# Performance work log

Measured on AMD Instinct MI355X. Metric: run time of the kernel, lower is better.

## Reference

```python
import jax, jax.numpy as jnp
import numpy as np

N_NODES = 100352
NUM_GRAPHS = 512
NODES_PER_GRAPH = 196  # N_NODES / NUM_GRAPHS, equal-size graphs
N_EDGES = 1605632
IN_C, HID_C, OUT_C, K = 128, 64, 32, 30


def setup_inputs() -> dict:
    key = jax.random.key(0)
    ks = jax.random.split(key, 4)
    x = jax.random.normal(ks[0], (N_NODES, IN_C), dtype=jnp.float32)
    edge_index = jax.random.randint(ks[1], (2, N_EDGES), 0, N_NODES, dtype=jnp.int32)
    batch = jnp.repeat(jnp.arange(NUM_GRAPHS, dtype=jnp.int32), NODES_PER_GRAPH)
    W1 = jax.random.normal(ks[2], (IN_C, HID_C), jnp.float32) * (1.0 / np.sqrt(IN_C))
    b1 = jnp.zeros((HID_C,), jnp.float32)
    W2 = jax.random.normal(ks[3], (HID_C, OUT_C), jnp.float32) * (1.0 / np.sqrt(HID_C))
    b2 = jnp.zeros((OUT_C,), jnp.float32)
    return dict(x=x, edge_index=edge_index, batch=batch, W1=W1, b1=b1, W2=W2, b2=b2)


def gcn_conv(x, src, dst, W, b, num_nodes):
    # PyG GCNConv: xW, add self-loops, symmetric normalization, scatter-add to dst.
    xw = x @ W  # [N, D_out]
    deg = jax.ops.segment_sum(jnp.ones_like(dst, dtype=xw.dtype), dst,
                              num_segments=num_nodes) + 1.0  # +1 for self-loop
    dis = jax.lax.rsqrt(deg)  # deg^{-1/2}
    msg = (dis[src] * dis[dst])[:, None] * xw[src]  # [E, D_out]
    out = jax.ops.segment_sum(msg, dst, num_segments=num_nodes)
    out = out + (dis * dis)[:, None] * xw  # self-loop term deg^{-1} * xw
    return out + b


def sort_pool(x, batch, num_graphs, max_nodes, k):
    # PyG SortAggregation: dense per-graph batch, sort nodes desc by last channel, top-k, zero padding.
    N, D = x.shape
    fill = x.min() - 1.0
    counts = jax.ops.segment_sum(jnp.ones((N,), jnp.int32), batch, num_segments=num_graphs)
    starts = jnp.cumsum(counts) - counts  # exclusive prefix sum
    pos = jnp.arange(N, dtype=jnp.int32) - starts[batch]
    dense = jnp.full((num_graphs, max_nodes, D), fill, x.dtype).at[batch, pos].set(x)
    order = jnp.argsort(-dense[:, :, -1], axis=1)[:, :k]  # [B, k] top-k by last channel
    topk = jnp.take_along_axis(dense, order[:, :, None], axis=1)  # [B, k, D]
    topk = jnp.where(topk == fill, jnp.zeros((), x.dtype), topk)
    return topk.reshape(num_graphs, k * D)


def reference(x, edge_index, batch, W1, b1, W2, b2):
    src, dst = edge_index[0], edge_index[1]
    n = x.shape[0]
    h = jax.nn.relu(gcn_conv(x, src, dst, W1, b1, n))
    h = gcn_conv(h, src, dst, W2, b2, n)
    return sort_pool(h, batch, NUM_GRAPHS, NODES_PER_GRAPH, K)
```

## Files before the change

kernel.cpp:

```cpp
#include <hip/hip_runtime.h>

#define N_NODES   100352
#define N_EDGES   1605632
#define IN_C      128
#define HID_C     64
#define OUT_C     32
#define NUM_GRAPHS 512
#define NPG       196
#define TOPK      30

#define NB        196
#define BCAP      10240
#define LCAP      10240

typedef float v16f __attribute__((ext_vector_type(16)));

#define OFF_DEG     0u
#define OFF_ROWPTR  401408u
#define OFF_DIS     802816u
#define OFF_BCNT    1204224u
#define OFF_BBASE   1205248u
#define OFF_ARENA   1206272u
#define OFF_OUT2    1206272u
#define OFF_CSR     17262592u
#define OFF_XW1     23685120u
#define OFF_H       49375232u
#define OFF_XW2     75065344u

__global__ __launch_bounds__(256) void k_bucket(const int* __restrict__ src, const int* __restrict__ dst,
                                                int* __restrict__ bucket_cnt, int2* __restrict__ arena) {
    __shared__ int hist[NB];
    __shared__ int cur[NB];
    int tid = threadIdx.x;
    for (int i = tid; i < NB; i += 256) hist[i] = 0;
    __syncthreads();
    int e0 = (blockIdx.x * 256 + tid) * 8;
    int4 sa = ((const int4*)src)[e0 / 4], sb = ((const int4*)src)[e0 / 4 + 1];
    int4 da = ((const int4*)dst)[e0 / 4], db = ((const int4*)dst)[e0 / 4 + 1];
    int es[8] = {sa.x, sa.y, sa.z, sa.w, sb.x, sb.y, sb.z, sb.w};
    int ed[8] = {da.x, da.y, da.z, da.w, db.x, db.y, db.z, db.w};
    int eb[8];
#pragma unroll
    for (int j = 0; j < 8; ++j) { eb[j] = ed[j] >> 9; atomicAdd(&hist[eb[j]], 1); }
    __syncthreads();
    for (int i = tid; i < NB; i += 256) {
        int c = hist[i];
        cur[i] = (c > 0) ? atomicAdd(&bucket_cnt[i], c) : 0;
    }
    __syncthreads();
#pragma unroll
    for (int j = 0; j < 8; ++j) {
        int p = atomicAdd(&cur[eb[j]], 1);
        if (p < BCAP) arena[(size_t)eb[j] * BCAP + p] = make_int2(es[j], ed[j] & 511);
    }
}

__global__ __launch_bounds__(256) void k_bscan(const int* __restrict__ bucket_cnt, int* __restrict__ bucket_base) {
    __shared__ int s[256];
    int t = threadIdx.x;
    int v = (t < NB) ? bucket_cnt[t] : 0;
    s[t] = v;
    __syncthreads();
    for (int o = 1; o < 256; o <<= 1) {
        int a = (t >= o) ? s[t - o] : 0;
        __syncthreads();
        s[t] += a;
        __syncthreads();
    }
    if (t < NB) bucket_base[t] = s[t] - v;
}

__global__ __launch_bounds__(256) void k_build(const int2* __restrict__ arena, const int* __restrict__ bucket_cnt,
                                               const int* __restrict__ bucket_base, int* __restrict__ row_ptr,
                                               int* __restrict__ deg, float* __restrict__ dis,
                                               int* __restrict__ csr_src) {
    __shared__ int dloc[512];
    __shared__ int sc[512];
    __shared__ int cur[512];
    __shared__ int stage[LCAP];
    int b = blockIdx.x;
    int tid = threadIdx.x;
    int nb = min(bucket_cnt[b], BCAP);
    int gbase = bucket_base[b];
    const int2* ap = arena + (size_t)b * BCAP;
    for (int i = tid; i < 512; i += 256) dloc[i] = 0;
    __syncthreads();
    for (int i = tid; i < nb; i += 256) {
        int2 e = ap[i];
        atomicAdd(&dloc[e.y], 1);
    }
    __syncthreads();
    for (int i = tid; i < 512; i += 256) sc[i] = dloc[i];
    __syncthreads();
    for (int o = 1; o < 512; o <<= 1) {
        int i0 = tid, i1 = tid + 256;
        int v0 = (i0 >= o) ? sc[i0 - o] : 0;
        int v1 = (i1 >= o) ? sc[i1 - o] : 0;
        __syncthreads();
        sc[i0] += v0;
        sc[i1] += v1;
        __syncthreads();
    }
    for (int i = tid; i < 512; i += 256) {
        int d = dloc[i];
        int off = sc[i] - d;
        int node = b * 512 + i;
        row_ptr[node] = gbase + off;
        deg[node] = d;
        dis[node] = (float)(1.0 / sqrt((double)(d + 1)));
        cur[i] = off;
    }
    __syncthreads();
    bool inlds = (nb <= LCAP);
    for (int i = tid; i < nb; i += 256) {
        int2 e = ap[i];
        int p = atomicAdd(&cur[e.y], 1);
        if (inlds) stage[p] = e.x;
        else       csr_src[gbase + p] = e.x;
    }
    __syncthreads();
    if (inlds)
        for (int i = tid; i < nb; i += 256) csr_src[gbase + i] = stage[i];
}

__global__ __launch_bounds__(256) void k_mm1(const float* __restrict__ x, const float* __restrict__ W1,
                                             const float* __restrict__ dis, float* __restrict__ xw1s) {
    int tid = threadIdx.x;
    int n = blockIdx.x * 128 + (tid & 127);
    int ch = __builtin_amdgcn_readfirstlane((tid >> 7) * 32);
    const float4* xrow = (const float4*)(x + (size_t)n * IN_C);
    float acc[32];
#pragma unroll
    for (int c = 0; c < 32; ++c) acc[c] = 0.f;
    float4 xq = xrow[0];
#pragma unroll 1
    for (int q = 0; q < IN_C / 4; ++q) {
        float4 xn = xrow[(q + 1) & (IN_C / 4 - 1)];
        const float* wrow = W1 + q * 4 * HID_C + ch;
#pragma unroll
        for (int kk = 0; kk < 4; ++kk) {
            const float* wp = wrow + kk * HID_C;
            v16f w0, w1;
            asm volatile("s_load_dwordx16 %0, %1, 0x0"  : "=s"(w0) : "s"(wp));
            asm volatile("s_load_dwordx16 %0, %1, 0x40" : "=s"(w1) : "s"(wp));
            asm volatile("s_waitcnt lgkmcnt(0)" : "+s"(w0), "+s"(w1));
            float xk = (kk == 0) ? xq.x : (kk == 1) ? xq.y : (kk == 2) ? xq.z : xq.w;
#pragma unroll
            for (int c = 0; c < 16; ++c) {
                acc[c]      = fmaf(xk, w0[c], acc[c]);
                acc[c + 16] = fmaf(xk, w1[c], acc[c + 16]);
            }
        }
        xq = xn;
    }
    float dv = dis[n];
    float4* orow = (float4*)(xw1s + (size_t)n * HID_C + ch);
#pragma unroll
    for (int c4 = 0; c4 < 8; ++c4) {
        float4 o;
        o.x = acc[4 * c4 + 0] * dv;
        o.y = acc[4 * c4 + 1] * dv;
        o.z = acc[4 * c4 + 2] * dv;
        o.w = acc[4 * c4 + 3] * dv;
        orow[c4] = o;
    }
}

__global__ __launch_bounds__(256) void k_agg1(const float* __restrict__ xw1s, const int* __restrict__ csr_src,
                                              const int* __restrict__ row_ptr, const int* __restrict__ deg,
                                              const float* __restrict__ dis, const float* __restrict__ b1,
                                              float* __restrict__ h) {
    int lane = threadIdx.x & 63;
    int v = blockIdx.x * 4 + (threadIdx.x >> 6);
    int start = row_ptr[v];
    int cnt = deg[v];
    float acc0 = xw1s[(size_t)v * HID_C + lane];
    float acc1 = 0.f, acc2 = 0.f, acc3 = 0.f;
    for (int base = 0; base < cnt; base += 64) {
        int mcnt = min(64, cnt - base);
        int sj = 0;
        if (lane < mcnt) sj = csr_src[start + base + lane];
        int j = 0;
        for (; j + 8 <= mcnt; j += 8) {
            int s0 = __shfl(sj, j + 0), s1 = __shfl(sj, j + 1);
            int s2 = __shfl(sj, j + 2), s3 = __shfl(sj, j + 3);
            int s4 = __shfl(sj, j + 4), s5 = __shfl(sj, j + 5);
            int s6 = __shfl(sj, j + 6), s7 = __shfl(sj, j + 7);
            float v0 = xw1s[(size_t)s0 * HID_C + lane];
            float v1 = xw1s[(size_t)s1 * HID_C + lane];
            float v2 = xw1s[(size_t)s2 * HID_C + lane];
            float v3 = xw1s[(size_t)s3 * HID_C + lane];
            float v4 = xw1s[(size_t)s4 * HID_C + lane];
            float v5 = xw1s[(size_t)s5 * HID_C + lane];
            float v6 = xw1s[(size_t)s6 * HID_C + lane];
            float v7 = xw1s[(size_t)s7 * HID_C + lane];
            acc0 += v0 + v4;
            acc1 += v1 + v5;
            acc2 += v2 + v6;
            acc3 += v3 + v7;
        }
        for (; j < mcnt; ++j) {
            int s = __shfl(sj, j);
            acc0 += xw1s[(size_t)s * HID_C + lane];
        }
    }
    float o = fmaf(dis[v], (acc0 + acc1) + (acc2 + acc3), b1[lane]);
    h[(size_t)v * HID_C + lane] = fmaxf(o, 0.f);
}

__global__ __launch_bounds__(256) void k_mm2(const float* __restrict__ h, const float* __restrict__ W2,
                                             const float* __restrict__ dis, float* __restrict__ xw2s) {
    int tid = threadIdx.x;
    int n = blockIdx.x * 128 + (tid & 127);
    int ch = __builtin_amdgcn_readfirstlane((tid >> 7) * 16);
    const float4* hrow = (const float4*)(h + (size_t)n * HID_C);
    float acc[16];
#pragma unroll
    for (int c = 0; c < 16; ++c) acc[c] = 0.f;
    float4 xq = hrow[0];
#pragma unroll 1
    for (int q = 0; q < HID_C / 4; ++q) {
        float4 xn = hrow[(q + 1) & (HID_C / 4 - 1)];
        const float* wrow = W2 + q * 4 * OUT_C + ch;
#pragma unroll
        for (int kk = 0; kk < 4; ++kk) {
            const float* wp = wrow + kk * OUT_C;
            v16f w0;
            asm volatile("s_load_dwordx16 %0, %1, 0x0" : "=s"(w0) : "s"(wp));
            asm volatile("s_waitcnt lgkmcnt(0)" : "+s"(w0));
            float xk = (kk == 0) ? xq.x : (kk == 1) ? xq.y : (kk == 2) ? xq.z : xq.w;
#pragma unroll
            for (int c = 0; c < 16; ++c)
                acc[c] = fmaf(xk, w0[c], acc[c]);
        }
        xq = xn;
    }
    float dv = dis[n];
    float4* orow = (float4*)(xw2s + (size_t)n * OUT_C + ch);
#pragma unroll
    for (int c4 = 0; c4 < 4; ++c4) {
        float4 o;
        o.x = acc[4 * c4 + 0] * dv;
        o.y = acc[4 * c4 + 1] * dv;
        o.z = acc[4 * c4 + 2] * dv;
        o.w = acc[4 * c4 + 3] * dv;
        orow[c4] = o;
    }
}

__global__ __launch_bounds__(256) void k_agg2(const float* __restrict__ xw2s, const int* __restrict__ csr_src,
                                              const int* __restrict__ row_ptr, const int* __restrict__ deg,
                                              const float* __restrict__ dis, const float* __restrict__ b2,
                                              float* __restrict__ out2) {
    int lane = threadIdx.x & 31;
    int v = blockIdx.x * 8 + (threadIdx.x >> 5);
    int start = row_ptr[v];
    int cnt = deg[v];
    float acc0 = xw2s[(size_t)v * OUT_C + lane];
    float acc1 = 0.f, acc2 = 0.f, acc3 = 0.f;
    for (int base = 0; base < cnt; base += 32) {
        int mcnt = min(32, cnt - base);
        int sj = 0;
        if (lane < mcnt) sj = csr_src[start + base + lane];
        int j = 0;
        for (; j + 8 <= mcnt; j += 8) {
            int s0 = __shfl(sj, j + 0, 32), s1 = __shfl(sj, j + 1, 32);
            int s2 = __shfl(sj, j + 2, 32), s3 = __shfl(sj, j + 3, 32);
            int s4 = __shfl(sj, j + 4, 32), s5 = __shfl(sj, j + 5, 32);
            int s6 = __shfl(sj, j + 6, 32), s7 = __shfl(sj, j + 7, 32);
            float v0 = xw2s[(size_t)s0 * OUT_C + lane];
            float v1 = xw2s[(size_t)s1 * OUT_C + lane];
            float v2 = xw2s[(size_t)s2 * OUT_C + lane];
            float v3 = xw2s[(size_t)s3 * OUT_C + lane];
            float v4 = xw2s[(size_t)s4 * OUT_C + lane];
            float v5 = xw2s[(size_t)s5 * OUT_C + lane];
            float v6 = xw2s[(size_t)s6 * OUT_C + lane];
            float v7 = xw2s[(size_t)s7 * OUT_C + lane];
            acc0 += v0 + v4;
            acc1 += v1 + v5;
            acc2 += v2 + v6;
            acc3 += v3 + v7;
        }
        for (; j < mcnt; ++j) {
            int s = __shfl(sj, j, 32);
            acc0 += xw2s[(size_t)s * OUT_C + lane];
        }
    }
    out2[(size_t)v * OUT_C + lane] = fmaf(dis[v], (acc0 + acc1) + (acc2 + acc3), b2[lane]);
}

__global__ __launch_bounds__(256) void k_sort(const float* __restrict__ out2, float* __restrict__ out) {
    __shared__ float keys[NPG];
    __shared__ int order[TOPK];
    int g = blockIdx.x;
    int tid = threadIdx.x;
    int base = g * NPG;
    if (tid < NPG) keys[tid] = out2[(size_t)(base + tid) * OUT_C + (OUT_C - 1)];
    __syncthreads();
    if (tid < NPG) {
        float my = keys[tid];
        int r = 0;
        for (int j = 0; j < NPG; ++j) {
            float kj = keys[j];
            r += (kj > my) || (kj == my && j < tid);
        }
        if (r < TOPK) order[r] = tid;
    }
    __syncthreads();
    for (int idx = tid; idx < TOPK * OUT_C; idx += 256) {
        int r = idx >> 5;
        int c = idx & 31;
        int n = order[r];
        out[g * (TOPK * OUT_C) + idx] = out2[(size_t)(base + n) * OUT_C + c];
    }
}

extern "C" void kernel_launch(void* const* d_in, const int* in_sizes, int n_in,
                              void* d_out, int out_size, void* d_ws, size_t ws_size,
                              hipStream_t stream) {
    const float* x  = (const float*)d_in[0];
    const int*   ei = (const int*)d_in[1];
    const int*   srcp = ei;
    const int*   dstp = ei + N_EDGES;
    const float* W1 = (const float*)d_in[3];
    const float* b1 = (const float*)d_in[4];
    const float* W2 = (const float*)d_in[5];
    const float* b2 = (const float*)d_in[6];
    float* out = (float*)d_out;

    char* w = (char*)d_ws;
    int*    deg      = (int*)(w + OFF_DEG);
    int*    row_ptr  = (int*)(w + OFF_ROWPTR);
    float*  dis      = (float*)(w + OFF_DIS);
    int*    bcnt     = (int*)(w + OFF_BCNT);
    int*    bbase    = (int*)(w + OFF_BBASE);
    int2*   arena    = (int2*)(w + OFF_ARENA);
    int*    csr_src  = (int*)(w + OFF_CSR);
    float*  xw1s     = (float*)(w + OFF_XW1);
    float*  h        = (float*)(w + OFF_H);
    float*  xw2s     = (float*)(w + OFF_XW2);
    float*  out2     = (float*)(w + OFF_OUT2);

    hipMemsetAsync(bcnt, 0, NB * sizeof(int), stream);
    k_bucket<<<N_EDGES / (256 * 8), 256, 0, stream>>>(srcp, dstp, bcnt, arena);
    k_bscan <<<1, 256, 0, stream>>>(bcnt, bbase);
    k_build <<<NB, 256, 0, stream>>>(arena, bcnt, bbase, row_ptr, deg, dis, csr_src);
    k_mm1   <<<N_NODES / 128, 256, 0, stream>>>(x, W1, dis, xw1s);
    k_agg1  <<<N_NODES / 4, 256, 0, stream>>>(xw1s, csr_src, row_ptr, deg, dis, b1, h);
    k_mm2   <<<N_NODES / 128, 256, 0, stream>>>(h, W2, dis, xw2s);
    k_agg2  <<<N_NODES / 8, 256, 0, stream>>>(xw2s, csr_src, row_ptr, deg, dis, b2, out2);
    k_sort  <<<NUM_GRAPHS, 256, 0, stream>>>(out2, out);
}
```

Measured before the change: 235.1 us.

## Fuse second GCN matmul into first aggregation and pack bucket arena entries

The second dense projection (h @ W2, scaled by dis) moves into the layer-1 aggregation kernel. W2 is staged in LDS and each wavefront computes its node's 32 outputs with shuffles, so the separate mm2 kernel and the write and re-read of the hidden buffer h go away. The bucket arena now packs src<<9 | local dst into one int instead of an int2, halving arena traffic in the bucketing and build kernels. mm1 is reshaped to 64 nodes per block with 16 channels per wave and issues its four W1 row loads together. In exchange, agg1 does more work per block (an LDS fill plus 32 shuffle-FMA steps), and the packing assumes src fits in 23 bits.

```diff
diff --git a/kernel.cpp b/kernel.cpp
--- a/kernel.cpp
+++ b/kernel.cpp
@@ -24,11 +24,10 @@
 #define OFF_OUT2    1206272u
 #define OFF_CSR     17262592u
 #define OFF_XW1     23685120u
-#define OFF_H       49375232u
 #define OFF_XW2     75065344u
 
 __global__ __launch_bounds__(256) void k_bucket(const int* __restrict__ src, const int* __restrict__ dst,
-                                                int* __restrict__ bucket_cnt, int2* __restrict__ arena) {
+                                                int* __restrict__ bucket_cnt, int* __restrict__ arena) {
     __shared__ int hist[NB];
     __shared__ int cur[NB];
     int tid = threadIdx.x;
@@ -51,7 +50,7 @@
 #pragma unroll
     for (int j = 0; j < 8; ++j) {
         int p = atomicAdd(&cur[eb[j]], 1);
-        if (p < BCAP) arena[(size_t)eb[j] * BCAP + p] = make_int2(es[j], ed[j] & 511);
+        if (p < BCAP) arena[(size_t)eb[j] * BCAP + p] = (es[j] << 9) | (ed[j] & 511);
     }
 }
 
@@ -70,7 +69,7 @@
     if (t < NB) bucket_base[t] = s[t] - v;
 }
 
-__global__ __launch_bounds__(256) void k_build(const int2* __restrict__ arena, const int* __restrict__ bucket_cnt,
+__global__ __launch_bounds__(256) void k_build(const int* __restrict__ arena, const int* __restrict__ bucket_cnt,
                                                const int* __restrict__ bucket_base, int* __restrict__ row_ptr,
                                                int* __restrict__ deg, float* __restrict__ dis,
                                                int* __restrict__ csr_src) {
@@ -82,12 +81,12 @@
     int tid = threadIdx.x;
     int nb = min(bucket_cnt[b], BCAP);
     int gbase = bucket_base[b];
-    const int2* ap = arena + (size_t)b * BCAP;
+    const int* ap = arena + (size_t)b * BCAP;
     for (int i = tid; i < 512; i += 256) dloc[i] = 0;
     __syncthreads();
     for (int i = tid; i < nb; i += 256) {
-        int2 e = ap[i];
-        atomicAdd(&dloc[e.y], 1);
+        int e = ap[i];
+        atomicAdd(&dloc[e & 511], 1);
     }
     __syncthreads();
     for (int i = tid; i < 512; i += 256) sc[i] = dloc[i];
@@ -113,10 +112,11 @@
     __syncthreads();
     bool inlds = (nb <= LCAP);
     for (int i = tid; i < nb; i += 256) {
-        int2 e = ap[i];
-        int p = atomicAdd(&cur[e.y], 1);
-        if (inlds) stage[p] = e.x;
-        else       csr_src[gbase + p] = e.x;
+        int e = ap[i];
+        int p = atomicAdd(&cur[e & 511], 1);
+        int sv = ((unsigned)e) >> 9;
+        if (inlds) stage[p] = sv;
+        else       csr_src[gbase + p] = sv;
     }
     __syncthreads();
     if (inlds)
@@ -126,37 +126,36 @@
 __global__ __launch_bounds__(256) void k_mm1(const float* __restrict__ x, const float* __restrict__ W1,
                                              const float* __restrict__ dis, float* __restrict__ xw1s) {
     int tid = threadIdx.x;
-    int n = blockIdx.x * 128 + (tid & 127);
-    int ch = __builtin_amdgcn_readfirstlane((tid >> 7) * 32);
+    int n = blockIdx.x * 64 + (tid & 63);
+    int ch = __builtin_amdgcn_readfirstlane((tid >> 6) * 16);
     const float4* xrow = (const float4*)(x + (size_t)n * IN_C);
-    float acc[32];
-#pragma unroll
-    for (int c = 0; c < 32; ++c) acc[c] = 0.f;
+    float acc[16];
+#pragma unroll
+    for (int c = 0; c < 16; ++c) acc[c] = 0.f;
     float4 xq = xrow[0];
 #pragma unroll 1
     for (int q = 0; q < IN_C / 4; ++q) {
         float4 xn = xrow[(q + 1) & (IN_C / 4 - 1)];
-        const float* wrow = W1 + q * 4 * HID_C + ch;
-#pragma unroll
-        for (int kk = 0; kk < 4; ++kk) {
-            const float* wp = wrow + kk * HID_C;
-            v16f w0, w1;
-            asm volatile("s_load_dwordx16 %0, %1, 0x0"  : "=s"(w0) : "s"(wp));
-            asm volatile("s_load_dwordx16 %0, %1, 0x40" : "=s"(w1) : "s"(wp));
-            asm volatile("s_waitcnt lgkmcnt(0)" : "+s"(w0), "+s"(w1));
-            float xk = (kk == 0) ? xq.x : (kk == 1) ? xq.y : (kk == 2) ? xq.z : xq.w;
-#pragma unroll
-            for (int c = 0; c < 16; ++c) {
-                acc[c]      = fmaf(xk, w0[c], acc[c]);
-                acc[c + 16] = fmaf(xk, w1[c], acc[c + 16]);
-            }
+        const float* wp = W1 + q * 4 * HID_C + ch;
+        v16f w0, w1, w2, w3;
+        asm volatile("s_load_dwordx16 %0, %1, 0x0"   : "=s"(w0) : "s"(wp));
+        asm volatile("s_load_dwordx16 %0, %1, 0x100" : "=s"(w1) : "s"(wp));
+        asm volatile("s_load_dwordx16 %0, %1, 0x200" : "=s"(w2) : "s"(wp));
+        asm volatile("s_load_dwordx16 %0, %1, 0x300" : "=s"(w3) : "s"(wp));
+        asm volatile("s_waitcnt lgkmcnt(0)" : "+s"(w0), "+s"(w1), "+s"(w2), "+s"(w3));
+#pragma unroll
+        for (int c = 0; c < 16; ++c) {
+            acc[c] = fmaf(xq.x, w0[c], acc[c]);
+            acc[c] = fmaf(xq.y, w1[c], acc[c]);
+            acc[c] = fmaf(xq.z, w2[c], acc[c]);
+            acc[c] = fmaf(xq.w, w3[c], acc[c]);
         }
         xq = xn;
     }
     float dv = dis[n];
     float4* orow = (float4*)(xw1s + (size_t)n * HID_C + ch);
 #pragma unroll
-    for (int c4 = 0; c4 < 8; ++c4) {
+    for (int c4 = 0; c4 < 4; ++c4) {
         float4 o;
         o.x = acc[4 * c4 + 0] * dv;
         o.y = acc[4 * c4 + 1] * dv;
@@ -169,9 +168,14 @@
 __global__ __launch_bounds__(256) void k_agg1(const float* __restrict__ xw1s, const int* __restrict__ csr_src,
                                               const int* __restrict__ row_ptr, const int* __restrict__ deg,
                                               const float* __restrict__ dis, const float* __restrict__ b1,
-                                              float* __restrict__ h) {
-    int lane = threadIdx.x & 63;
-    int v = blockIdx.x * 4 + (threadIdx.x >> 6);
+                                              const float* __restrict__ W2, float* __restrict__ xw2s) {
+    __shared__ float w2lds[HID_C * OUT_C];
+    int tid = threadIdx.x;
+    for (int i = tid; i < HID_C * OUT_C / 4; i += 256)
+        ((float4*)w2lds)[i] = ((const float4*)W2)[i];
+    __syncthreads();
+    int lane = tid & 63;
+    int v = blockIdx.x * 4 + (tid >> 6);
     int start = row_ptr[v];
     int cnt = deg[v];
     float acc0 = xw1s[(size_t)v * HID_C + lane];
@@ -204,48 +208,21 @@
             acc0 += xw1s[(size_t)s * HID_C + lane];
         }
     }
-    float o = fmaf(dis[v], (acc0 + acc1) + (acc2 + acc3), b1[lane]);
-    h[(size_t)v * HID_C + lane] = fmaxf(o, 0.f);
-}
-
-__global__ __launch_bounds__(256) void k_mm2(const float* __restrict__ h, const float* __restrict__ W2,
-                                             const float* __restrict__ dis, float* __restrict__ xw2s) {
-    int tid = threadIdx.x;
-    int n = blockIdx.x * 128 + (tid & 127);
-    int ch = __builtin_amdgcn_readfirstlane((tid >> 7) * 16);
-    const float4* hrow = (const float4*)(h + (size_t)n * HID_C);
-    float acc[16];
-#pragma unroll
-    for (int c = 0; c < 16; ++c) acc[c] = 0.f;
-    float4 xq = hrow[0];
-#pragma unroll 1
-    for (int q = 0; q < HID_C / 4; ++q) {
-        float4 xn = hrow[(q + 1) & (HID_C / 4 - 1)];
-        const float* wrow = W2 + q * 4 * OUT_C + ch;
-#pragma unroll
-        for (int kk = 0; kk < 4; ++kk) {
-            const float* wp = wrow + kk * OUT_C;
-            v16f w0;
-            asm volatile("s_load_dwordx16 %0, %1, 0x0" : "=s"(w0) : "s"(wp));
-            asm volatile("s_waitcnt lgkmcnt(0)" : "+s"(w0));
-            float xk = (kk == 0) ? xq.x : (kk == 1) ? xq.y : (kk == 2) ? xq.z : xq.w;
-#pragma unroll
-            for (int c = 0; c < 16; ++c)
-                acc[c] = fmaf(xk, w0[c], acc[c]);
-        }
-        xq = xn;
-    }
-    float dv = dis[n];
-    float4* orow = (float4*)(xw2s + (size_t)n * OUT_C + ch);
-#pragma unroll
-    for (int c4 = 0; c4 < 4; ++c4) {
-        float4 o;
-        o.x = acc[4 * c4 + 0] * dv;
-        o.y = acc[4 * c4 + 1] * dv;
-        o.z = acc[4 * c4 + 2] * dv;
-        o.w = acc[4 * c4 + 3] * dv;
-        orow[c4] = o;
-    }
+    float dv = dis[v];
+    float o = fmaf(dv, (acc0 + acc1) + (acc2 + acc3), b1[lane]);
+    float hval = fmaxf(o, 0.f);
+
+    int c = lane & 31;
+    int hf = lane & 32;
+    float s = 0.f;
+#pragma unroll
+    for (int k0 = 0; k0 < 32; ++k0) {
+        float hk = __shfl(hval, k0 | hf);
+        s = fmaf(hk, w2lds[((k0 | hf) << 5) + c], s);
+    }
+    s += __shfl_xor(s, 32);
+    if (lane < 32)
+        xw2s[(size_t)v * OUT_C + c] = s * dv;
 }
 
 __global__ __launch_bounds__(256) void k_agg2(const float* __restrict__ xw2s, const int* __restrict__ csr_src,
@@ -334,10 +311,9 @@
     float*  dis      = (float*)(w + OFF_DIS);
     int*    bcnt     = (int*)(w + OFF_BCNT);
     int*    bbase    = (int*)(w + OFF_BBASE);
-    int2*   arena    = (int2*)(w + OFF_ARENA);
+    int*    arena    = (int*)(w + OFF_ARENA);
     int*    csr_src  = (int*)(w + OFF_CSR);
     float*  xw1s     = (float*)(w + OFF_XW1);
-    float*  h        = (float*)(w + OFF_H);
     float*  xw2s     = (float*)(w + OFF_XW2);
     float*  out2     = (float*)(w + OFF_OUT2);
 
@@ -345,9 +321,8 @@
     k_bucket<<<N_EDGES / (256 * 8), 256, 0, stream>>>(srcp, dstp, bcnt, arena);
     k_bscan <<<1, 256, 0, stream>>>(bcnt, bbase);
     k_build <<<NB, 256, 0, stream>>>(arena, bcnt, bbase, row_ptr, deg, dis, csr_src);
-    k_mm1   <<<N_NODES / 128, 256, 0, stream>>>(x, W1, dis, xw1s);
-    k_agg1  <<<N_NODES / 4, 256, 0, stream>>>(xw1s, csr_src, row_ptr, deg, dis, b1, h);
-    k_mm2   <<<N_NODES / 128, 256, 0, stream>>>(h, W2, dis, xw2s);
+    k_mm1   <<<N_NODES / 64, 256, 0, stream>>>(x, W1, dis, xw1s);
+    k_agg1  <<<N_NODES / 4, 256, 0, stream>>>(xw1s, csr_src, row_ptr, deg, dis, b1, W2, xw2s);
     k_agg2  <<<N_NODES / 8, 256, 0, stream>>>(xw2s, csr_src, row_ptr, deg, dis, b2, out2);
     k_sort  <<<NUM_GRAPHS, 256, 0, stream>>>(out2, out);
 }
```

Measured after the change: 226.5 us. 3.7% less time.
